# Kernel tuning notes

Measured on AMD Instinct MI355X. Metric: run time of the kernel, lower is better.

Reference implementation:

```python
import jax, jax.numpy as jnp
import numpy as np

N = 100000

def _gcn_layer(x, W, b, row, col, n):
    # x: [N, Fin] -> lin -> [N, Fout]
    h = x @ W + b
    # degree over row (includes self loops), dtype follows x
    deg = jnp.zeros((n,), dtype=h.dtype).at[row].add(jnp.ones_like(row, dtype=h.dtype))
    dis = deg ** -0.5
    norm = dis[row] * dis[col]                      # [E]
    msg = norm[:, None] * h[row]                    # gather + scale: [E, Fout]
    return jax.ops.segment_sum(msg, col, num_segments=n)  # scatter-add at targets


def setup_inputs() -> dict:
    key = jax.random.key(0)
    ks = jax.random.split(key, 10)
    x = jax.random.normal(ks[0], (N, 32), dtype=jnp.float32)
    feat = jax.random.normal(ks[1], (N, 32), dtype=jnp.float32)
    edge_index = jax.random.randint(ks[2], (2, 1600000), 0, N, dtype=jnp.int64)
    # params (torch Linear stored as [in, out] here; y = x @ W + b)
    def lin(k, fin, fout):
        s = 1.0 / np.sqrt(fin)
        kw, kb = jax.random.split(k)
        W = jax.random.uniform(kw, (fin, fout), minval=-s, maxval=s, dtype=jnp.float32)
        b = jax.random.uniform(kb, (fout,), minval=-s, maxval=s, dtype=jnp.float32)
        return W, b
    W1, b1 = lin(ks[3], 64, 64)
    W2, b2 = lin(ks[4], 64, 64)
    Wfc, bfc = lin(ks[5], 64, 64)
    return {"x": x, "feat": feat, "edge_index": edge_index,
            "W1": W1, "b1": b1, "W2": W2, "b2": b2, "Wfc": Wfc, "bfc": bfc}


def reference(x, feat, edge_index, W1, b1, W2, b2, Wfc, bfc):
    n = x.shape[0]
    h = jnp.concatenate([x, feat], axis=-1)          # [N, 64]
    # add self loops once (same augmented edge set used by every layer)
    loops = jnp.arange(n, dtype=edge_index.dtype)
    row = jnp.concatenate([edge_index[0], loops])
    col = jnp.concatenate([edge_index[1], loops])
    h = jax.nn.relu(_gcn_layer(h, W1, b1, row, col, n))
    h = jax.nn.relu(_gcn_layer(h, W2, b2, row, col, n))
    return jax.nn.relu(h @ Wfc + bfc)                # [N, 64]
```

## Files before the change

kernel.cpp:

```cpp
#include <hip/hip_runtime.h>
#include <hip/hip_bf16.h>


#define FDIM 64
#define NPART 4
#define GPB 64
#define NB 256
#define BW 512
#define MAXP 1024
#define GPLIN 1024

typedef __hip_bfloat16 bf16;
typedef short v8s __attribute__((ext_vector_type(8)));
typedef float v4f __attribute__((ext_vector_type(4)));

static __device__ __forceinline__ float ulo2f(unsigned u) {
    union { unsigned x; float f; } v; v.x = u << 16; return v.f;
}
static __device__ __forceinline__ float uhi2f(unsigned u) {
    union { unsigned x; float f; } v; v.x = u & 0xFFFF0000u; return v.f;
}
static __device__ __forceinline__ unsigned f2bu(float f) {
    bf16 b = __float2bfloat16(f);
    return (unsigned)(*(unsigned short*)&b);
}

__global__ __launch_bounds__(1024)
void k_hd(const int* __restrict__ row, unsigned* __restrict__ part,
          int E, int n, int psize, int psize4) {
    __shared__ unsigned sm[6256];
    int t = threadIdx.x, b = blockIdx.x;
    int p = b >> 6, g = b & 63;
    int base = p * psize;
    int lim = n - base; if (lim > psize) lim = psize;
    int lim4 = (lim + 3) >> 2;
    for (int i = t; i < lim4; i += 1024) sm[i] = 0u;
    __syncthreads();
    for (int e = (g * 1024 + t) * 4; e < E; e += GPB * 4096) {
        int4 r4 = *(const int4*)&row[e];
        int r0 = r4.x - base, r1 = r4.y - base, r2 = r4.z - base, r3 = r4.w - base;
        if ((unsigned)r0 < (unsigned)lim) atomicAdd(&sm[r0 >> 2], 1u << ((r0 & 3) * 8));
        if ((unsigned)r1 < (unsigned)lim) atomicAdd(&sm[r1 >> 2], 1u << ((r1 & 3) * 8));
        if ((unsigned)r2 < (unsigned)lim) atomicAdd(&sm[r2 >> 2], 1u << ((r2 & 3) * 8));
        if ((unsigned)r3 < (unsigned)lim) atomicAdd(&sm[r3 >> 2], 1u << ((r3 & 3) * 8));
    }
    __syncthreads();
    unsigned* dst = part + ((size_t)p * GPB + g) * psize4;
    for (int i = t; i < lim4; i += 1024) dst[i] = sm[i];
}

__global__ __launch_bounds__(1024)
void k_hc(const int* __restrict__ col, int* __restrict__ M,
          int E, int P, int CH) {
    __shared__ int h[MAXP];
    int t = threadIdx.x, cb = blockIdx.x;
    for (int i = t; i < P; i += 1024) h[i] = 0;
    __syncthreads();
    int s = cb * CH, e = min(s + CH, E);
    for (int i = s + t * 4; i < e; i += 4096) {
        int4 c4 = *(const int4*)&col[i];
        atomicAdd(&h[c4.x >> 9], 1);
        atomicAdd(&h[c4.y >> 9], 1);
        atomicAdd(&h[c4.z >> 9], 1);
        atomicAdd(&h[c4.w >> 9], 1);
    }
    __syncthreads();
    for (int p = t; p < P; p += 1024) M[p * NB + cb] = h[p];
}

__global__ void k_ds1(const unsigned* __restrict__ part, float* __restrict__ dis,
                      int* __restrict__ M, int* __restrict__ bsum,
                      int n, int psize4, int ndis4, int P) {
    __shared__ int sc[256];
    int t = threadIdx.x, b = blockIdx.x;
    if (b < ndis4) {
        int i4 = b * 256 + t;
        int i = i4 * 4;
        if (i >= n) return;
        int p = i4 / psize4, loc = i4 - p * psize4;
        const unsigned* src = part + (size_t)p * GPB * psize4 + loc;
        unsigned s0 = 0, s1 = 0, s2 = 0, s3 = 0;
        #pragma unroll 8
        for (int g = 0; g < GPB; ++g) {
            unsigned u = src[(size_t)g * psize4];
            s0 += u & 255u; s1 += (u >> 8) & 255u;
            s2 += (u >> 16) & 255u; s3 += u >> 24;
        }
        dis[i] = rsqrtf((float)s0 + 1.0f);
        if (i + 1 < n) dis[i + 1] = rsqrtf((float)s1 + 1.0f);
        if (i + 2 < n) dis[i + 2] = rsqrtf((float)s2 + 1.0f);
        if (i + 3 < n) dis[i + 3] = rsqrtf((float)s3 + 1.0f);
    } else {
        int sb = b - ndis4;
        int i = sb * 256 + t;
        int v = M[i];
        sc[t] = v;
        __syncthreads();
        for (int d = 1; d < 256; d <<= 1) {
            int u = (t >= d) ? sc[t - d] : 0;
            __syncthreads(); sc[t] += u; __syncthreads();
        }
        M[i] = sc[t] - v;
        if (t == 255) bsum[sb] = sc[255];
    }
}

__global__ __launch_bounds__(1024)
void k_csc(const int* __restrict__ row, const int* __restrict__ col,
           const int* __restrict__ M, const int* __restrict__ bsum,
           int* __restrict__ s4, int E, int CH, int P) {
    __shared__ int sc[256];
    __shared__ int bs[256];
    __shared__ int cur[MAXP];
    int t = threadIdx.x, b = blockIdx.x;
    if (t < 256) { int v = (t < P) ? bsum[t] : 0; sc[t] = v; bs[t] = v; }
    __syncthreads();
    for (int d = 1; d < 256; d <<= 1) {
        int u = (t < 256 && t >= d) ? sc[t - d] : 0;
        __syncthreads();
        if (t < 256) sc[t] += u;
        __syncthreads();
    }
    if (t < 256) bs[t] = sc[t] - bs[t];
    __syncthreads();
    for (int p = t; p < P; p += 1024) cur[p] = bs[p] + M[p * NB + b];
    __syncthreads();
    int s = b * CH, e = min(s + CH, E);
    for (int i = s + t * 4; i < e; i += 4096) {
        int4 r4 = *(const int4*)&row[i];
        int4 c4 = *(const int4*)&col[i];
        int p0 = atomicAdd(&cur[c4.x >> 9], 1);
        s4[p0] = (r4.x << 9) | (c4.x & 511);
        int p1 = atomicAdd(&cur[c4.y >> 9], 1);
        s4[p1] = (r4.y << 9) | (c4.y & 511);
        int p2 = atomicAdd(&cur[c4.z >> 9], 1);
        s4[p2] = (r4.z << 9) | (c4.z & 511);
        int p3 = atomicAdd(&cur[c4.w >> 9], 1);
        s4[p3] = (r4.w << 9) | (c4.w & 511);
    }
}

__global__ __launch_bounds__(1024)
void k_fsort(const int* __restrict__ s4, const int* __restrict__ bsum,
             int* __restrict__ rows4, int* __restrict__ off,
             int n, int E, int P) {
    __shared__ int sc[256];
    __shared__ int bs[256];
    __shared__ int hist[BW];
    __shared__ int loff[BW];
    __shared__ int tmp[256];
    int t = threadIdx.x, b = blockIdx.x;
    if (t < 256) { int v = (t < P) ? bsum[t] : 0; sc[t] = v; bs[t] = v; }
    __syncthreads();
    for (int d = 1; d < 256; d <<= 1) {
        int u = (t < 256 && t >= d) ? sc[t - d] : 0;
        __syncthreads();
        if (t < 256) sc[t] += u;
        __syncthreads();
    }
    if (t < 256) bs[t] = sc[t] - bs[t];
    __syncthreads();
    int gs = bs[b];
    int ge = gs + bsum[b];
    int c0 = b << 9;
    int lim = n - c0; if (lim > BW) lim = BW;
    for (int i = t; i < BW; i += 1024) hist[i] = 0;
    __syncthreads();
    for (int i = gs + t; i < ge; i += 1024)
        atomicAdd(&hist[s4[i] & 511], 1);
    __syncthreads();
    int s0 = 0, s1v = 0, ps = 0;
    if (t < 256) {
        s0 = hist[2 * t]; s1v = hist[2 * t + 1];
        ps = s0 + s1v;
        tmp[t] = ps;
    }
    __syncthreads();
    for (int d = 1; d < 256; d <<= 1) {
        int u = (t < 256 && t >= d) ? tmp[t - d] : 0;
        __syncthreads();
        if (t < 256) tmp[t] += u;
        __syncthreads();
    }
    if (t < 256) {
        int ex = tmp[t] - ps;
        loff[2 * t] = ex;
        loff[2 * t + 1] = ex + s0;
    }
    __syncthreads();
    for (int i = t; i < lim; i += 1024) off[c0 + i] = gs + loff[i];
    if (b == P - 1 && t == 0) off[n] = E;
    __syncthreads();
    for (int i = gs + t; i < ge; i += 1024) {
        int v2 = s4[i];
        int pos = gs + atomicAdd(&loff[v2 & 511], 1);
        rows4[pos] = v2 >> 9;
    }
}

__global__ __launch_bounds__(256, 4)
void k_linc(const float* __restrict__ x, const float* __restrict__ feat,
            const float* __restrict__ W, const float* __restrict__ bvec,
            const float* __restrict__ dis, bf16* __restrict__ g1, int n) {
    __shared__ float sIn[4][FDIM];
    int t = threadIdx.x;
    int local = t >> 6, j = t & 63;
    float Wreg[FDIM];
    #pragma unroll
    for (int k = 0; k < FDIM; ++k) Wreg[k] = W[k * FDIM + j];
    float bj = bvec[j];
    int gw = blockIdx.x * 4 + local;
    int nwl = GPLIN * 4;
    for (int w = gw; w < n; w += nwl) {
        sIn[local][j] = (j < 32) ? x[(size_t)w * 32 + j]
                                 : feat[(size_t)w * 32 + (j - 32)];
        __threadfence_block();
        float o = bj;
        #pragma unroll
        for (int k4 = 0; k4 < 16; ++k4) {
            float4 h4 = *(const float4*)&sIn[local][k4 * 4];
            o = fmaf(h4.x, Wreg[4 * k4 + 0], o);
            o = fmaf(h4.y, Wreg[4 * k4 + 1], o);
            o = fmaf(h4.z, Wreg[4 * k4 + 2], o);
            o = fmaf(h4.w, Wreg[4 * k4 + 3], o);
        }
        g1[(size_t)w * FDIM + j] = __float2bfloat16(dis[w] * o);
        __threadfence_block();
    }
}

__global__ __launch_bounds__(256, 8)
void k_gather(const int* __restrict__ rows4, const int* __restrict__ off,
              const float* __restrict__ dis, const bf16* __restrict__ g,
              bf16* __restrict__ a, int n) {
    int t = blockIdx.x * blockDim.x + threadIdx.x;
    int w = t >> 6;
    if (w >= n) return;
    int lane = threadIdx.x & 63;
    int h = lane >> 5;
    int j2 = lane & 31;
    const unsigned* g32 = (const unsigned*)g;
    float acc0 = 0.0f, acc1 = 0.0f;
    int s = off[w], e = off[w + 1];
    int k = s;
    for (; k + 16 <= e; k += 16) {
        #pragma unroll
        for (int i = 0; i < 8; ++i) {
            int r = rows4[k + 2 * i + h];
            unsigned u = g32[(size_t)r * 32 + j2];
            acc0 += ulo2f(u);
            acc1 += uhi2f(u);
        }
    }
    if (k < e) {
        #pragma unroll
        for (int i = 0; i < 8; ++i) {
            int idx = k + 2 * i + h;
            int r = rows4[min(idx, e - 1)];
            unsigned u = g32[(size_t)r * 32 + j2];
            float wg = (idx < e) ? 1.0f : 0.0f;
            acc0 = fmaf(wg, ulo2f(u), acc0);
            acc1 = fmaf(wg, uhi2f(u), acc1);
        }
    }
    acc0 += __shfl_xor(acc0, 32, 64);
    acc1 += __shfl_xor(acc1, 32, 64);
    if (h == 0) {
        unsigned su = g32[(size_t)w * 32 + j2];
        float dv = dis[w];
        float v0 = fmaxf(dv * (acc0 + ulo2f(su)), 0.0f);
        float v1 = fmaxf(dv * (acc1 + uhi2f(su)), 0.0f);
        ((unsigned*)a)[(size_t)w * 32 + j2] = f2bu(v0) | (f2bu(v1) << 16);
    }
}

template <bool FINAL>
__global__ __launch_bounds__(256, 4)
void k_mat(const bf16* __restrict__ A, const float* __restrict__ W,
           const float* __restrict__ bvec, const float* __restrict__ dis,
           void* __restrict__ outp, int n) {
    __shared__ __align__(16) bf16 sWt[FDIM * FDIM];
    int t = threadIdx.x;
    for (int idx = t; idx < FDIM * FDIM; idx += 256) {
        int kk = idx >> 6, nn = idx & 63;
        sWt[nn * FDIM + kk] = __float2bfloat16(W[idx]);
    }
    __syncthreads();
    int wave = t >> 6, lane = t & 63;
    int quad = lane >> 4, l15 = lane & 15;
    v8s bfr[4][2];
    #pragma unroll
    for (int nt = 0; nt < 4; ++nt) {
        #pragma unroll
        for (int kf = 0; kf < 2; ++kf)
            bfr[nt][kf] = *(const v8s*)&sWt[(nt * 16 + l15) * FDIM + kf * 32 + quad * 8];
    }
    float bj[4];
    #pragma unroll
    for (int nt = 0; nt < 4; ++nt) bj[nt] = bvec[nt * 16 + l15];

    int ntiles = (n + 15) >> 4;
    int step = gridDim.x * 4;
    for (int tile = blockIdx.x * 4 + wave; tile < ntiles; tile += step) {
        int m0 = tile << 4;
        int mA = m0 + l15; if (mA >= n) mA = n - 1;
        v8s af0 = *(const v8s*)&A[(size_t)mA * FDIM + quad * 8];
        v8s af1 = *(const v8s*)&A[(size_t)mA * FDIM + 32 + quad * 8];
        v4f acc[4];
        #pragma unroll
        for (int nt = 0; nt < 4; ++nt) {
            acc[nt] = (v4f){0.f, 0.f, 0.f, 0.f};
            acc[nt] = __builtin_amdgcn_mfma_f32_16x16x32_bf16(af0, bfr[nt][0], acc[nt], 0, 0, 0);
            acc[nt] = __builtin_amdgcn_mfma_f32_16x16x32_bf16(af1, bfr[nt][1], acc[nt], 0, 0, 0);
        }
        #pragma unroll
        for (int r = 0; r < 4; ++r) {
            int node = m0 + quad * 4 + r;
            if (node >= n) continue;
            float dv = FINAL ? 0.0f : dis[node];
            #pragma unroll
            for (int nt = 0; nt < 4; ++nt) {
                int j = nt * 16 + l15;
                float o = acc[nt][r] + bj[nt];
                if (FINAL) ((float*)outp)[(size_t)node * FDIM + j] = fmaxf(o, 0.0f);
                else ((bf16*)outp)[(size_t)node * FDIM + j] = __float2bfloat16(dv * o);
            }
        }
    }
}

extern "C" void kernel_launch(void* const* d_in, const int* in_sizes, int n_in,
                              void* d_out, int out_size, void* d_ws, size_t ws_size,
                              hipStream_t stream) {
    const float* x    = (const float*)d_in[0];
    const float* feat = (const float*)d_in[1];
    const int*   ei   = (const int*)d_in[2];
    const float* W1   = (const float*)d_in[3];
    const float* b1   = (const float*)d_in[4];
    const float* W2   = (const float*)d_in[5];
    const float* b2   = (const float*)d_in[6];
    const float* Wfc  = (const float*)d_in[7];
    const float* bfc  = (const float*)d_in[8];
    float* out = (float*)d_out;

    const int n = in_sizes[0] / 32;
    const int E = in_sizes[2] / 2;
    const int* row = ei;
    const int* col = ei + E;

    const int psize = (((n + NPART - 1) / NPART) + 3) & ~3;
    const int psize4 = psize >> 2;
    const int P  = (n + BW - 1) / BW;
    const int CH = (((E + NB - 1) / NB) + 3) & ~3;
    const int total = P * NB;
    const int ndis4 = (((n + 3) / 4) + 255) / 256;

    int*   off  = (int*)d_ws;
    float* dis  = (float*)(off + (size_t)n + 1);
    int*   M    = (int*)(dis + n);
    int*   bsum = M + (size_t)total;
    int*   s4    = bsum + 256;
    int*   rows4 = s4 + E;
    size_t co = (size_t)(rows4 + E - (int*)d_ws);
    co = (co + 3) & ~(size_t)3;
    bf16*  bufA  = (bf16*)((int*)d_ws + co);
    bf16*  bufB  = bufA + (size_t)n * FDIM;
    unsigned* part = (unsigned*)bufA;

    k_hd<<<NPART * GPB, 1024, 0, stream>>>(row, part, E, n, psize, psize4);
    k_hc<<<NB, 1024, 0, stream>>>(col, M, E, P, CH);
    k_ds1<<<ndis4 + P, 256, 0, stream>>>(part, dis, M, bsum, n, psize4, ndis4, P);
    k_csc<<<NB, 1024, 0, stream>>>(row, col, M, bsum, s4, E, CH, P);
    k_fsort<<<P, 1024, 0, stream>>>(s4, bsum, rows4, off, n, E, P);
    k_linc<<<GPLIN, 256, 0, stream>>>(x, feat, W1, b1, dis, bufA, n);
    k_gather<<<(n + 3) / 4, 256, 0, stream>>>(rows4, off, dis, bufA, bufB, n);
    k_mat<false><<<512, 256, 0, stream>>>(bufB, W2, b2, dis, bufA, n);
    k_gather<<<(n + 3) / 4, 256, 0, stream>>>(rows4, off, dis, bufA, bufB, n);
    k_mat<true><<<512, 256, 0, stream>>>(bufB, Wfc, bfc, dis, out, n);
}
```

Before: 274.7 us.

## Fuse gather with MFMA matmul and merge histogram kernels

Merges the row-degree and column-bucket histogram kernels into one launch whose blocks branch on index. Fuses each neighbor gather/aggregation with the following 64x64 bf16 MFMA linear layer: each block gathers 16 nodes into shared memory, then each wave computes one 16-column slice. This drops the intermediate bufB round trip and two launches. In exchange the gather now runs with fixed 2048 blocks, adds __syncthreads per tile and gives each wave one node at a time, which may reduce memory-level parallelism in the latency-bound gather.

```diff
diff --git a/kernel.cpp b/kernel.cpp
--- a/kernel.cpp
+++ b/kernel.cpp
@@ -26,46 +26,45 @@
 }
 
 __global__ __launch_bounds__(1024)
-void k_hd(const int* __restrict__ row, unsigned* __restrict__ part,
-          int E, int n, int psize, int psize4) {
+void k_h2(const int* __restrict__ row, const int* __restrict__ col,
+          unsigned* __restrict__ part, int* __restrict__ M,
+          int E, int n, int psize, int psize4, int P, int CH) {
     __shared__ unsigned sm[6256];
     int t = threadIdx.x, b = blockIdx.x;
-    int p = b >> 6, g = b & 63;
-    int base = p * psize;
-    int lim = n - base; if (lim > psize) lim = psize;
-    int lim4 = (lim + 3) >> 2;
-    for (int i = t; i < lim4; i += 1024) sm[i] = 0u;
-    __syncthreads();
-    for (int e = (g * 1024 + t) * 4; e < E; e += GPB * 4096) {
-        int4 r4 = *(const int4*)&row[e];
-        int r0 = r4.x - base, r1 = r4.y - base, r2 = r4.z - base, r3 = r4.w - base;
-        if ((unsigned)r0 < (unsigned)lim) atomicAdd(&sm[r0 >> 2], 1u << ((r0 & 3) * 8));
-        if ((unsigned)r1 < (unsigned)lim) atomicAdd(&sm[r1 >> 2], 1u << ((r1 & 3) * 8));
-        if ((unsigned)r2 < (unsigned)lim) atomicAdd(&sm[r2 >> 2], 1u << ((r2 & 3) * 8));
-        if ((unsigned)r3 < (unsigned)lim) atomicAdd(&sm[r3 >> 2], 1u << ((r3 & 3) * 8));
-    }
-    __syncthreads();
-    unsigned* dst = part + ((size_t)p * GPB + g) * psize4;
-    for (int i = t; i < lim4; i += 1024) dst[i] = sm[i];
-}
-
-__global__ __launch_bounds__(1024)
-void k_hc(const int* __restrict__ col, int* __restrict__ M,
-          int E, int P, int CH) {
-    __shared__ int h[MAXP];
-    int t = threadIdx.x, cb = blockIdx.x;
-    for (int i = t; i < P; i += 1024) h[i] = 0;
-    __syncthreads();
-    int s = cb * CH, e = min(s + CH, E);
-    for (int i = s + t * 4; i < e; i += 4096) {
-        int4 c4 = *(const int4*)&col[i];
-        atomicAdd(&h[c4.x >> 9], 1);
-        atomicAdd(&h[c4.y >> 9], 1);
-        atomicAdd(&h[c4.z >> 9], 1);
-        atomicAdd(&h[c4.w >> 9], 1);
-    }
-    __syncthreads();
-    for (int p = t; p < P; p += 1024) M[p * NB + cb] = h[p];
+    if (b < NPART * GPB) {
+        int p = b >> 6, g = b & 63;
+        int base = p * psize;
+        int lim = n - base; if (lim > psize) lim = psize;
+        int lim4 = (lim + 3) >> 2;
+        for (int i = t; i < lim4; i += 1024) sm[i] = 0u;
+        __syncthreads();
+        for (int e = (g * 1024 + t) * 4; e < E; e += GPB * 4096) {
+            int4 r4 = *(const int4*)&row[e];
+            int r0 = r4.x - base, r1 = r4.y - base, r2 = r4.z - base, r3 = r4.w - base;
+            if ((unsigned)r0 < (unsigned)lim) atomicAdd(&sm[r0 >> 2], 1u << ((r0 & 3) * 8));
+            if ((unsigned)r1 < (unsigned)lim) atomicAdd(&sm[r1 >> 2], 1u << ((r1 & 3) * 8));
+            if ((unsigned)r2 < (unsigned)lim) atomicAdd(&sm[r2 >> 2], 1u << ((r2 & 3) * 8));
+            if ((unsigned)r3 < (unsigned)lim) atomicAdd(&sm[r3 >> 2], 1u << ((r3 & 3) * 8));
+        }
+        __syncthreads();
+        unsigned* dst = part + ((size_t)p * GPB + g) * psize4;
+        for (int i = t; i < lim4; i += 1024) dst[i] = sm[i];
+    } else {
+        int cb = b - NPART * GPB;
+        int* h = (int*)sm;
+        for (int i = t; i < P; i += 1024) h[i] = 0;
+        __syncthreads();
+        int s = cb * CH, e = min(s + CH, E);
+        for (int i = s + t * 4; i < e; i += 4096) {
+            int4 c4 = *(const int4*)&col[i];
+            atomicAdd(&h[c4.x >> 9], 1);
+            atomicAdd(&h[c4.y >> 9], 1);
+            atomicAdd(&h[c4.z >> 9], 1);
+            atomicAdd(&h[c4.w >> 9], 1);
+        }
+        __syncthreads();
+        for (int p = t; p < P; p += 1024) M[p * NB + cb] = h[p];
+    }
 }
 
 __global__ void k_ds1(const unsigned* __restrict__ part, float* __restrict__ dis,
@@ -229,103 +228,88 @@
     }
 }
 
-__global__ __launch_bounds__(256, 8)
-void k_gather(const int* __restrict__ rows4, const int* __restrict__ off,
-              const float* __restrict__ dis, const bf16* __restrict__ g,
-              bf16* __restrict__ a, int n) {
-    int t = blockIdx.x * blockDim.x + threadIdx.x;
-    int w = t >> 6;
-    if (w >= n) return;
-    int lane = threadIdx.x & 63;
-    int h = lane >> 5;
-    int j2 = lane & 31;
-    const unsigned* g32 = (const unsigned*)g;
-    float acc0 = 0.0f, acc1 = 0.0f;
-    int s = off[w], e = off[w + 1];
-    int k = s;
-    for (; k + 16 <= e; k += 16) {
-        #pragma unroll
-        for (int i = 0; i < 8; ++i) {
-            int r = rows4[k + 2 * i + h];
-            unsigned u = g32[(size_t)r * 32 + j2];
-            acc0 += ulo2f(u);
-            acc1 += uhi2f(u);
-        }
-    }
-    if (k < e) {
-        #pragma unroll
-        for (int i = 0; i < 8; ++i) {
-            int idx = k + 2 * i + h;
-            int r = rows4[min(idx, e - 1)];
-            unsigned u = g32[(size_t)r * 32 + j2];
-            float wg = (idx < e) ? 1.0f : 0.0f;
-            acc0 = fmaf(wg, ulo2f(u), acc0);
-            acc1 = fmaf(wg, uhi2f(u), acc1);
-        }
-    }
-    acc0 += __shfl_xor(acc0, 32, 64);
-    acc1 += __shfl_xor(acc1, 32, 64);
-    if (h == 0) {
-        unsigned su = g32[(size_t)w * 32 + j2];
-        float dv = dis[w];
-        float v0 = fmaxf(dv * (acc0 + ulo2f(su)), 0.0f);
-        float v1 = fmaxf(dv * (acc1 + uhi2f(su)), 0.0f);
-        ((unsigned*)a)[(size_t)w * 32 + j2] = f2bu(v0) | (f2bu(v1) << 16);
-    }
-}
-
 template <bool FINAL>
 __global__ __launch_bounds__(256, 4)
-void k_mat(const bf16* __restrict__ A, const float* __restrict__ W,
-           const float* __restrict__ bvec, const float* __restrict__ dis,
-           void* __restrict__ outp, int n) {
+void k_gm(const int* __restrict__ rows4, const int* __restrict__ off,
+          const float* __restrict__ dis, const bf16* __restrict__ g,
+          const float* __restrict__ W, const float* __restrict__ bvec,
+          void* __restrict__ outp, int n) {
     __shared__ __align__(16) bf16 sWt[FDIM * FDIM];
+    __shared__ __align__(16) unsigned sA[16 * 36];
     int t = threadIdx.x;
     for (int idx = t; idx < FDIM * FDIM; idx += 256) {
         int kk = idx >> 6, nn = idx & 63;
         sWt[nn * FDIM + kk] = __float2bfloat16(W[idx]);
     }
     __syncthreads();
-    int wave = t >> 6, lane = t & 63;
+    int wv = t >> 6, lane = t & 63;
     int quad = lane >> 4, l15 = lane & 15;
-    v8s bfr[4][2];
-    #pragma unroll
-    for (int nt = 0; nt < 4; ++nt) {
+    int h = lane >> 5, j2 = lane & 31;
+    v8s bfr0 = *(const v8s*)&sWt[(wv * 16 + l15) * FDIM + quad * 8];
+    v8s bfr1 = *(const v8s*)&sWt[(wv * 16 + l15) * FDIM + 32 + quad * 8];
+    float bj = bvec[wv * 16 + l15];
+    const unsigned* g32 = (const unsigned*)g;
+    const bf16* sAb = (const bf16*)sA;
+    int ntiles = (n + 15) >> 4;
+    for (int tile = blockIdx.x; tile < ntiles; tile += gridDim.x) {
+        int m0 = tile << 4;
         #pragma unroll
-        for (int kf = 0; kf < 2; ++kf)
-            bfr[nt][kf] = *(const v8s*)&sWt[(nt * 16 + l15) * FDIM + kf * 32 + quad * 8];
-    }
-    float bj[4];
-    #pragma unroll
-    for (int nt = 0; nt < 4; ++nt) bj[nt] = bvec[nt * 16 + l15];
-
-    int ntiles = (n + 15) >> 4;
-    int step = gridDim.x * 4;
-    for (int tile = blockIdx.x * 4 + wave; tile < ntiles; tile += step) {
-        int m0 = tile << 4;
-        int mA = m0 + l15; if (mA >= n) mA = n - 1;
-        v8s af0 = *(const v8s*)&A[(size_t)mA * FDIM + quad * 8];
-        v8s af1 = *(const v8s*)&A[(size_t)mA * FDIM + 32 + quad * 8];
-        v4f acc[4];
-        #pragma unroll
-        for (int nt = 0; nt < 4; ++nt) {
-            acc[nt] = (v4f){0.f, 0.f, 0.f, 0.f};
-            acc[nt] = __builtin_amdgcn_mfma_f32_16x16x32_bf16(af0, bfr[nt][0], acc[nt], 0, 0, 0);
-            acc[nt] = __builtin_amdgcn_mfma_f32_16x16x32_bf16(af1, bfr[nt][1], acc[nt], 0, 0, 0);
-        }
+        for (int i = 0; i < 4; ++i) {
+            int w = m0 + wv * 4 + i;
+            if (w >= n) break;
+            float acc0 = 0.0f, acc1 = 0.0f;
+            int s = off[w], e = off[w + 1];
+            int k = s;
+            for (; k + 16 <= e; k += 16) {
+                #pragma unroll
+                for (int u = 0; u < 8; ++u) {
+                    int r = rows4[k + 2 * u + h];
+                    unsigned uu = g32[(size_t)r * 32 + j2];
+                    acc0 += ulo2f(uu);
+                    acc1 += uhi2f(uu);
+                }
+            }
+            if (k < e) {
+                #pragma unroll
+                for (int u = 0; u < 8; ++u) {
+                    int idx = k + 2 * u + h;
+                    int r = rows4[min(idx, e - 1)];
+                    unsigned uu = g32[(size_t)r * 32 + j2];
+                    float wg = (idx < e) ? 1.0f : 0.0f;
+                    acc0 = fmaf(wg, ulo2f(uu), acc0);
+                    acc1 = fmaf(wg, uhi2f(uu), acc1);
+                }
+            }
+            acc0 += __shfl_xor(acc0, 32, 64);
+            acc1 += __shfl_xor(acc1, 32, 64);
+            if (h == 0) {
+                unsigned su = g32[(size_t)w * 32 + j2];
+                float dv = dis[w];
+                float v0 = fmaxf(dv * (acc0 + ulo2f(su)), 0.0f);
+                float v1 = fmaxf(dv * (acc1 + uhi2f(su)), 0.0f);
+                sA[(wv * 4 + i) * 36 + j2] = f2bu(v0) | (f2bu(v1) << 16);
+            }
+        }
+        __syncthreads();
+        v8s af0 = *(const v8s*)&sAb[l15 * 72 + quad * 8];
+        v8s af1 = *(const v8s*)&sAb[l15 * 72 + 32 + quad * 8];
+        v4f acc = (v4f){0.f, 0.f, 0.f, 0.f};
+        acc = __builtin_amdgcn_mfma_f32_16x16x32_bf16(af0, bfr0, acc, 0, 0, 0);
+        acc = __builtin_amdgcn_mfma_f32_16x16x32_bf16(af1, bfr1, acc, 0, 0, 0);
         #pragma unroll
         for (int r = 0; r < 4; ++r) {
             int node = m0 + quad * 4 + r;
             if (node >= n) continue;
-            float dv = FINAL ? 0.0f : dis[node];
-            #pragma unroll
-            for (int nt = 0; nt < 4; ++nt) {
-                int j = nt * 16 + l15;
-                float o = acc[nt][r] + bj[nt];
-                if (FINAL) ((float*)outp)[(size_t)node * FDIM + j] = fmaxf(o, 0.0f);
-                else ((bf16*)outp)[(size_t)node * FDIM + j] = __float2bfloat16(dv * o);
+            int j = wv * 16 + l15;
+            float o = acc[r] + bj;
+            if (FINAL) {
+                ((float*)outp)[(size_t)node * FDIM + j] = fmaxf(o, 0.0f);
+            } else {
+                ((bf16*)outp)[(size_t)node * FDIM + j] =
+                    __float2bfloat16(dis[node] * o);
             }
         }
+        __syncthreads();
     }
 }
 
@@ -367,14 +351,12 @@
     bf16*  bufB  = bufA + (size_t)n * FDIM;
     unsigned* part = (unsigned*)bufA;
 
-    k_hd<<<NPART * GPB, 1024, 0, stream>>>(row, part, E, n, psize, psize4);
-    k_hc<<<NB, 1024, 0, stream>>>(col, M, E, P, CH);
+    k_h2<<<NPART * GPB + NB, 1024, 0, stream>>>(row, col, part, M, E, n,
+                                                psize, psize4, P, CH);
     k_ds1<<<ndis4 + P, 256, 0, stream>>>(part, dis, M, bsum, n, psize4, ndis4, P);
     k_csc<<<NB, 1024, 0, stream>>>(row, col, M, bsum, s4, E, CH, P);
     k_fsort<<<P, 1024, 0, stream>>>(s4, bsum, rows4, off, n, E, P);
     k_linc<<<GPLIN, 256, 0, stream>>>(x, feat, W1, b1, dis, bufA, n);
-    k_gather<<<(n + 3) / 4, 256, 0, stream>>>(rows4, off, dis, bufA, bufB, n);
-    k_mat<false><<<512, 256, 0, stream>>>(bufB, W2, b2, dis, bufA, n);
-    k_gather<<<(n + 3) / 4, 256, 0, stream>>>(rows4, off, dis, bufA, bufB, n);
-    k_mat<true><<<512, 256, 0, stream>>>(bufB, Wfc, bfc, dis, out, n);
-}
+    k_gm<false><<<2048, 256, 0, stream>>>(rows4, off, dis, bufA, W2, b2, bufB, n);
+    k_gm<true><<<2048, 256, 0, stream>>>(rows4, off, dis, bufB, Wfc, bfc, out, n);
+}
```

After: 295.7 us. 7.6% more time.
